# Performance work log

Hardware: AMD Instinct MI355X
Metric: run time of the kernel (lower is better)

## Reference

```python
import jax, jax.numpy as jnp
import numpy as np

# HEAD_ORDER column indices: predictor=0, cf_perm=1, cf_primary=2, cf_secondary=3, reorder=4, interleave=5
# emb rows follow sorted(used_heads) = ['cf_perm','cf_primary','cf_secondary','predictor','reorder']
_HEAD_ROW = {'cf_perm': 0, 'cf_primary': 1, 'cf_secondary': 2, 'predictor': 3, 'reorder': 4}
_HEAD_COL = {'predictor': 0, 'cf_perm': 1, 'cf_primary': 2, 'cf_secondary': 3, 'reorder': 4, 'interleave': 5}
_PAIRS = [('predictor', 'cf_perm'), ('predictor', 'cf_primary'), ('predictor', 'cf_secondary'),
          ('reorder', 'cf_perm'), ('reorder', 'cf_primary'), ('reorder', 'cf_secondary')]
_SCALE = 1.0

BATCH, NEGS, INPUT_DIM, DIM, VOCAB, N_HEADS = 2048, 512, 256, 64, 32, 5


def setup_inputs() -> dict:
    key = jax.random.key(0)
    ks = jax.random.split(key, 5)
    x = jax.random.normal(ks[0], (BATCH, INPUT_DIM), dtype=jnp.float32)
    neg_labels = jax.random.randint(ks[1], (BATCH, NEGS, 6), 0, VOCAB, dtype=jnp.int64)
    emb = jax.random.normal(ks[2], (N_HEADS, VOCAB, DIM), dtype=jnp.float32)
    gate_w = jax.random.normal(ks[3], (6, DIM, INPUT_DIM), dtype=jnp.float32) * (INPUT_DIM ** -0.5)
    gate_b = jax.random.normal(ks[4], (6, DIM), dtype=jnp.float32) * 0.01
    return {'x': x, 'neg_labels': neg_labels, 'emb': emb, 'gate_w': gate_w, 'gate_b': gate_b}


def reference(x, neg_labels, emb, gate_w, gate_b):
    # gates for all 6 pairs at once: (6, batch, dim)
    g = jnp.tanh(jnp.einsum('bi,pdi->pbd', x, gate_w) + gate_b[:, None, :])
    score = jnp.zeros((neg_labels.shape[0], neg_labels.shape[1]), dtype=x.dtype)
    for p, (a, b) in enumerate(_PAIRS):
        ea = emb[_HEAD_ROW[a]][neg_labels[:, :, _HEAD_COL[a]]]  # (batch, negs, dim)
        eb = emb[_HEAD_ROW[b]][neg_labels[:, :, _HEAD_COL[b]]]  # (batch, negs, dim)
        score = score + jnp.einsum('bnd,bd,bnd->bn', ea, g[p], eb)
    return score * _SCALE
```

## Files before the change

kernel.cpp:

```cpp
#include <hip/hip_runtime.h>
#include <hip/hip_bf16.h>

typedef __bf16 bf16x8 __attribute__((ext_vector_type(8)));
typedef float f32x4 __attribute__((ext_vector_type(4)));

#define BATCH 2048
#define NEGS 512
#define IN_DIM 256
#define DIM 64
#define NGATE 384
#define EMB_LD 72
#define TAB_LD 33

__device__ inline bf16x8 cvt8(float4 f0, float4 f1) {
    bf16x8 r;
    r[0] = (__bf16)f0.x; r[1] = (__bf16)f0.y; r[2] = (__bf16)f0.z; r[3] = (__bf16)f0.w;
    r[4] = (__bf16)f1.x; r[5] = (__bf16)f1.y; r[6] = (__bf16)f1.z; r[7] = (__bf16)f1.w;
    return r;
}

__global__ __launch_bounds__(64) void gate_gemm_kernel(
    const float* __restrict__ x, const float* __restrict__ gw,
    const float* __restrict__ gb, float* __restrict__ g)
{
    const int l = threadIdx.x;
    const int lm = l & 15, lq = l >> 4;
    const int m0 = blockIdx.x * 32;
    const int n0 = blockIdx.y * 32;
    f32x4 acc[2][2] = {};

#pragma unroll
    for (int s = 0; s < 8; ++s) {
        const int k0 = s * 32 + lq * 8;
        bf16x8 af[2], bfr[2];
#pragma unroll
        for (int mh = 0; mh < 2; ++mh) {
            const float* p = x + (size_t)(m0 + mh * 16 + lm) * IN_DIM + k0;
            af[mh] = cvt8(*(const float4*)p, *(const float4*)(p + 4));
        }
#pragma unroll
        for (int nh = 0; nh < 2; ++nh) {
            const float* p = gw + (size_t)(n0 + nh * 16 + lm) * IN_DIM + k0;
            bfr[nh] = cvt8(*(const float4*)p, *(const float4*)(p + 4));
        }
#pragma unroll
        for (int mh = 0; mh < 2; ++mh)
#pragma unroll
            for (int nh = 0; nh < 2; ++nh)
                acc[mh][nh] = __builtin_amdgcn_mfma_f32_16x16x32_bf16(af[mh], bfr[nh], acc[mh][nh], 0, 0, 0);
    }

#pragma unroll
    for (int mh = 0; mh < 2; ++mh) {
#pragma unroll
        for (int nh = 0; nh < 2; ++nh) {
            const int gc = n0 + nh * 16 + lm;
            const float bias = gb[gc];
#pragma unroll
            for (int r = 0; r < 4; ++r) {
                const int gr = m0 + mh * 16 + lq * 4 + r;
                g[(size_t)gr * NGATE + gc] = tanhf(acc[mh][nh][r] + bias);
            }
        }
    }
}

__global__ __launch_bounds__(256) void table_score_kernel(
    const int* __restrict__ labels, const float* __restrict__ emb,
    const float* __restrict__ g, float* __restrict__ out)
{
    __shared__ __align__(16) __bf16 embs[5 * 32 * EMB_LD];
    __shared__ __align__(16) float tab[2 * 6 * 32 * TAB_LD];

    const int t = threadIdx.x;
    const int b0 = blockIdx.x * 2;

#pragma unroll
    for (int c = 0; c < 5; ++c) {
        const int j = t + c * 256;
        const int head = j >> 8;
        const int rem = j & 255;
        const int v = rem >> 3, q = rem & 7;
        const float4* src = (const float4*)(emb + (size_t)j * 8);
        bf16x8 val = cvt8(src[0], src[1]);
        *(bf16x8*)&embs[head * (32 * EMB_LD) + v * EMB_LD + q * 8] = val;
    }
    __syncthreads();

    const int w = t >> 6, l = t & 63;
    const int lm = l & 15, lq = l >> 4;

    for (int id = w; id < 12; id += 4) {
        const int bi = id / 6, p = id % 6;
        const int b = b0 + bi;
        const int arow = (p < 3) ? 3 : 4;
        const int crow = (p < 3) ? p : p - 3;
        f32x4 acc[2][2] = {};

#pragma unroll
        for (int s = 0; s < 2; ++s) {
            const int k0 = s * 32 + lq * 8;
            const float* gp = g + (size_t)b * NGATE + p * 64 + k0;
            const float4 g0 = *(const float4*)gp;
            const float4 g1 = *(const float4*)(gp + 4);

            bf16x8 bfr[2], afr[2];
#pragma unroll
            for (int nh = 0; nh < 2; ++nh)
                bfr[nh] = *(const bf16x8*)&embs[crow * (32 * EMB_LD) + (nh * 16 + lm) * EMB_LD + k0];
#pragma unroll
            for (int mh = 0; mh < 2; ++mh) {
                bf16x8 ea = *(const bf16x8*)&embs[arow * (32 * EMB_LD) + (mh * 16 + lm) * EMB_LD + k0];
                bf16x8 r;
                r[0] = (__bf16)((float)ea[0] * g0.x); r[1] = (__bf16)((float)ea[1] * g0.y);
                r[2] = (__bf16)((float)ea[2] * g0.z); r[3] = (__bf16)((float)ea[3] * g0.w);
                r[4] = (__bf16)((float)ea[4] * g1.x); r[5] = (__bf16)((float)ea[5] * g1.y);
                r[6] = (__bf16)((float)ea[6] * g1.z); r[7] = (__bf16)((float)ea[7] * g1.w);
                afr[mh] = r;
            }
#pragma unroll
            for (int mh = 0; mh < 2; ++mh)
#pragma unroll
                for (int nh = 0; nh < 2; ++nh)
                    acc[mh][nh] = __builtin_amdgcn_mfma_f32_16x16x32_bf16(afr[mh], bfr[nh], acc[mh][nh], 0, 0, 0);
        }

        float* tb = tab + id * (32 * TAB_LD);
#pragma unroll
        for (int mh = 0; mh < 2; ++mh)
#pragma unroll
            for (int nh = 0; nh < 2; ++nh) {
                const int col = nh * 16 + lm;
#pragma unroll
                for (int r = 0; r < 4; ++r)
                    tb[(mh * 16 + lq * 4 + r) * TAB_LD + col] = acc[mh][nh][r];
            }
    }
    __syncthreads();

#pragma unroll
    for (int bi = 0; bi < 2; ++bi) {
        const int b = b0 + bi;
        const int4* lp = (const int4*)(labels + (size_t)b * NEGS * 6) + 3 * t;
        const int4 q0 = lp[0];
        const int4 q1 = lp[1];
        const int4 q2 = lp[2];
        const float* tb = tab + bi * (6 * 32 * TAB_LD);

        const float sA =
            tb[0 * 32 * TAB_LD + q0.x * TAB_LD + q0.y] +
            tb[1 * 32 * TAB_LD + q0.x * TAB_LD + q0.z] +
            tb[2 * 32 * TAB_LD + q0.x * TAB_LD + q0.w] +
            tb[3 * 32 * TAB_LD + q1.x * TAB_LD + q0.y] +
            tb[4 * 32 * TAB_LD + q1.x * TAB_LD + q0.z] +
            tb[5 * 32 * TAB_LD + q1.x * TAB_LD + q0.w];
        const float sB =
            tb[0 * 32 * TAB_LD + q1.z * TAB_LD + q1.w] +
            tb[1 * 32 * TAB_LD + q1.z * TAB_LD + q2.x] +
            tb[2 * 32 * TAB_LD + q1.z * TAB_LD + q2.y] +
            tb[3 * 32 * TAB_LD + q2.z * TAB_LD + q1.w] +
            tb[4 * 32 * TAB_LD + q2.z * TAB_LD + q2.x] +
            tb[5 * 32 * TAB_LD + q2.z * TAB_LD + q2.y];

        float2 res; res.x = sA; res.y = sB;
        *(float2*)(out + (size_t)b * NEGS + 2 * t) = res;
    }
}

extern "C" void kernel_launch(void* const* d_in, const int* in_sizes, int n_in,
                              void* d_out, int out_size, void* d_ws, size_t ws_size,
                              hipStream_t stream) {
    const float* x      = (const float*)d_in[0];
    const int*   labels = (const int*)d_in[1];
    const float* emb    = (const float*)d_in[2];
    const float* gw     = (const float*)d_in[3];
    const float* gb     = (const float*)d_in[4];
    float* out = (float*)d_out;
    float* g   = (float*)d_ws;

    hipLaunchKernelGGL(gate_gemm_kernel, dim3(BATCH / 32, NGATE / 32), dim3(64), 0, stream,
                       x, gw, gb, g);
    hipLaunchKernelGGL(table_score_kernel, dim3(BATCH / 2), dim3(256), 0, stream,
                       labels, emb, g, out);
}
```

Measured before the change: 29.72 us.

## Store gates and score tables in bf16, retile gate GEMM, prefetch labels early

The gate GEMM now gives each wave one 16x16 tile, packs four waves per block, and writes the gates as bf16 instead of fp32. The score kernel loads labels and gates into registers before the embedding staging and barrier, so those global loads overlap the shared-memory setup. The per-pair score tables are stored in bf16, halving their LDS footprint, and occupancy is hinted to 3 blocks per CU. This cuts global and LDS traffic but adds bf16 rounding to the gate and table values, and the register prefetch raises register pressure.

Result: faster. 27.12 us (-8.8%).

```diff
diff --git a/kernel.cpp b/kernel.cpp
--- a/kernel.cpp
+++ b/kernel.cpp
@@ -7,10 +7,9 @@
 #define BATCH 2048
 #define NEGS 512
 #define IN_DIM 256
-#define DIM 64
 #define NGATE 384
 #define EMB_LD 72
-#define TAB_LD 33
+#define TAB_LD 34
 
 __device__ inline bf16x8 cvt8(float4 f0, float4 f1) {
     bf16x8 r;
@@ -19,80 +18,78 @@
     return r;
 }
 
-__global__ __launch_bounds__(64) void gate_gemm_kernel(
+__global__ __launch_bounds__(256) void gate_gemm_kernel(
     const float* __restrict__ x, const float* __restrict__ gw,
-    const float* __restrict__ gb, float* __restrict__ g)
+    const float* __restrict__ gb, __bf16* __restrict__ g)
 {
-    const int l = threadIdx.x;
+    const int w = threadIdx.x >> 6, l = threadIdx.x & 63;
     const int lm = l & 15, lq = l >> 4;
-    const int m0 = blockIdx.x * 32;
-    const int n0 = blockIdx.y * 32;
-    f32x4 acc[2][2] = {};
+    const int tile = blockIdx.x * 4 + w;
+    const int mt = tile / 24, nt = tile % 24;
+    const int m0 = mt * 16, n0 = nt * 16;
 
+    const float* xp = x + (size_t)(m0 + lm) * IN_DIM + lq * 8;
+    const float* wp = gw + (size_t)(n0 + lm) * IN_DIM + lq * 8;
+    f32x4 acc = {};
 #pragma unroll
     for (int s = 0; s < 8; ++s) {
-        const int k0 = s * 32 + lq * 8;
-        bf16x8 af[2], bfr[2];
+        bf16x8 a = cvt8(*(const float4*)(xp + s * 32), *(const float4*)(xp + s * 32 + 4));
+        bf16x8 b = cvt8(*(const float4*)(wp + s * 32), *(const float4*)(wp + s * 32 + 4));
+        acc = __builtin_amdgcn_mfma_f32_16x16x32_bf16(a, b, acc, 0, 0, 0);
+    }
+    const int col = n0 + lm;
+    const float bias = gb[col];
 #pragma unroll
-        for (int mh = 0; mh < 2; ++mh) {
-            const float* p = x + (size_t)(m0 + mh * 16 + lm) * IN_DIM + k0;
-            af[mh] = cvt8(*(const float4*)p, *(const float4*)(p + 4));
-        }
-#pragma unroll
-        for (int nh = 0; nh < 2; ++nh) {
-            const float* p = gw + (size_t)(n0 + nh * 16 + lm) * IN_DIM + k0;
-            bfr[nh] = cvt8(*(const float4*)p, *(const float4*)(p + 4));
-        }
-#pragma unroll
-        for (int mh = 0; mh < 2; ++mh)
-#pragma unroll
-            for (int nh = 0; nh < 2; ++nh)
-                acc[mh][nh] = __builtin_amdgcn_mfma_f32_16x16x32_bf16(af[mh], bfr[nh], acc[mh][nh], 0, 0, 0);
-    }
-
-#pragma unroll
-    for (int mh = 0; mh < 2; ++mh) {
-#pragma unroll
-        for (int nh = 0; nh < 2; ++nh) {
-            const int gc = n0 + nh * 16 + lm;
-            const float bias = gb[gc];
-#pragma unroll
-            for (int r = 0; r < 4; ++r) {
-                const int gr = m0 + mh * 16 + lq * 4 + r;
-                g[(size_t)gr * NGATE + gc] = tanhf(acc[mh][nh][r] + bias);
-            }
-        }
+    for (int r = 0; r < 4; ++r) {
+        const int row = m0 + lq * 4 + r;
+        g[(size_t)row * NGATE + col] = (__bf16)tanhf(acc[r] + bias);
     }
 }
 
-__global__ __launch_bounds__(256) void table_score_kernel(
+__global__ __launch_bounds__(256, 3) void table_score_kernel(
     const int* __restrict__ labels, const float* __restrict__ emb,
-    const float* __restrict__ g, float* __restrict__ out)
+    const __bf16* __restrict__ g, float* __restrict__ out)
 {
     __shared__ __align__(16) __bf16 embs[5 * 32 * EMB_LD];
-    __shared__ __align__(16) float tab[2 * 6 * 32 * TAB_LD];
+    __shared__ __align__(16) __bf16 tab[2 * 6 * 32 * TAB_LD];
 
     const int t = threadIdx.x;
     const int b0 = blockIdx.x * 2;
+    const int w = t >> 6, l = t & 63;
+    const int lm = l & 15, lq = l >> 4;
+
+    int4 q[2][3];
+#pragma unroll
+    for (int bi = 0; bi < 2; ++bi) {
+        const int4* lp = (const int4*)(labels + (size_t)(b0 + bi) * NEGS * 6) + 3 * t;
+        q[bi][0] = lp[0]; q[bi][1] = lp[1]; q[bi][2] = lp[2];
+    }
+    bf16x8 gv[3][2];
+#pragma unroll
+    for (int j = 0; j < 3; ++j) {
+        const int id = w + j * 4;
+        const int bi = id / 6, p = id % 6;
+        const __bf16* gp = g + (size_t)(b0 + bi) * NGATE + p * 64 + lq * 8;
+        gv[j][0] = *(const bf16x8*)gp;
+        gv[j][1] = *(const bf16x8*)(gp + 32);
+    }
 
 #pragma unroll
     for (int c = 0; c < 5; ++c) {
         const int j = t + c * 256;
         const int head = j >> 8;
         const int rem = j & 255;
-        const int v = rem >> 3, q = rem & 7;
+        const int v = rem >> 3, qq = rem & 7;
         const float4* src = (const float4*)(emb + (size_t)j * 8);
         bf16x8 val = cvt8(src[0], src[1]);
-        *(bf16x8*)&embs[head * (32 * EMB_LD) + v * EMB_LD + q * 8] = val;
+        *(bf16x8*)&embs[head * (32 * EMB_LD) + v * EMB_LD + qq * 8] = val;
     }
     __syncthreads();
 
-    const int w = t >> 6, l = t & 63;
-    const int lm = l & 15, lq = l >> 4;
-
-    for (int id = w; id < 12; id += 4) {
-        const int bi = id / 6, p = id % 6;
-        const int b = b0 + bi;
+#pragma unroll
+    for (int j = 0; j < 3; ++j) {
+        const int id = w + j * 4;
+        const int p = id % 6;
         const int arow = (p < 3) ? 3 : 4;
         const int crow = (p < 3) ? p : p - 3;
         f32x4 acc[2][2] = {};
@@ -100,9 +97,9 @@
 #pragma unroll
         for (int s = 0; s < 2; ++s) {
             const int k0 = s * 32 + lq * 8;
-            const float* gp = g + (size_t)b * NGATE + p * 64 + k0;
-            const float4 g0 = *(const float4*)gp;
-            const float4 g1 = *(const float4*)(gp + 4);
+            float gf[8];
+#pragma unroll
+            for (int i = 0; i < 8; ++i) gf[i] = (float)gv[j][s][i];
 
             bf16x8 bfr[2], afr[2];
 #pragma unroll
@@ -112,10 +109,8 @@
             for (int mh = 0; mh < 2; ++mh) {
                 bf16x8 ea = *(const bf16x8*)&embs[arow * (32 * EMB_LD) + (mh * 16 + lm) * EMB_LD + k0];
                 bf16x8 r;
-                r[0] = (__bf16)((float)ea[0] * g0.x); r[1] = (__bf16)((float)ea[1] * g0.y);
-                r[2] = (__bf16)((float)ea[2] * g0.z); r[3] = (__bf16)((float)ea[3] * g0.w);
-                r[4] = (__bf16)((float)ea[4] * g1.x); r[5] = (__bf16)((float)ea[5] * g1.y);
-                r[6] = (__bf16)((float)ea[6] * g1.z); r[7] = (__bf16)((float)ea[7] * g1.w);
+#pragma unroll
+                for (int i = 0; i < 8; ++i) r[i] = (__bf16)((float)ea[i] * gf[i]);
                 afr[mh] = r;
             }
 #pragma unroll
@@ -125,7 +120,7 @@
                     acc[mh][nh] = __builtin_amdgcn_mfma_f32_16x16x32_bf16(afr[mh], bfr[nh], acc[mh][nh], 0, 0, 0);
         }
 
-        float* tb = tab + id * (32 * TAB_LD);
+        __bf16* tb = tab + id * (32 * TAB_LD);
 #pragma unroll
         for (int mh = 0; mh < 2; ++mh)
 #pragma unroll
@@ -133,7 +128,7 @@
                 const int col = nh * 16 + lm;
 #pragma unroll
                 for (int r = 0; r < 4; ++r)
-                    tb[(mh * 16 + lq * 4 + r) * TAB_LD + col] = acc[mh][nh][r];
+                    tb[(mh * 16 + lq * 4 + r) * TAB_LD + col] = (__bf16)acc[mh][nh][r];
             }
     }
     __syncthreads();
@@ -141,26 +136,25 @@
 #pragma unroll
     for (int bi = 0; bi < 2; ++bi) {
         const int b = b0 + bi;
-        const int4* lp = (const int4*)(labels + (size_t)b * NEGS * 6) + 3 * t;
-        const int4 q0 = lp[0];
-        const int4 q1 = lp[1];
-        const int4 q2 = lp[2];
-        const float* tb = tab + bi * (6 * 32 * TAB_LD);
+        const int4 q0 = q[bi][0];
+        const int4 q1 = q[bi][1];
+        const int4 q2 = q[bi][2];
+        const __bf16* tb = tab + bi * (6 * 32 * TAB_LD);
 
         const float sA =
-            tb[0 * 32 * TAB_LD + q0.x * TAB_LD + q0.y] +
-            tb[1 * 32 * TAB_LD + q0.x * TAB_LD + q0.z] +
-            tb[2 * 32 * TAB_LD + q0.x * TAB_LD + q0.w] +
-            tb[3 * 32 * TAB_LD + q1.x * TAB_LD + q0.y] +
-            tb[4 * 32 * TAB_LD + q1.x * TAB_LD + q0.z] +
-            tb[5 * 32 * TAB_LD + q1.x * TAB_LD + q0.w];
+            (float)tb[0 * 32 * TAB_LD + q0.x * TAB_LD + q0.y] +
+            (float)tb[1 * 32 * TAB_LD + q0.x * TAB_LD + q0.z] +
+            (float)tb[2 * 32 * TAB_LD + q0.x * TAB_LD + q0.w] +
+            (float)tb[3 * 32 * TAB_LD + q1.x * TAB_LD + q0.y] +
+            (float)tb[4 * 32 * TAB_LD + q1.x * TAB_LD + q0.z] +
+            (float)tb[5 * 32 * TAB_LD + q1.x * TAB_LD + q0.w];
         const float sB =
-            tb[0 * 32 * TAB_LD + q1.z * TAB_LD + q1.w] +
-            tb[1 * 32 * TAB_LD + q1.z * TAB_LD + q2.x] +
-            tb[2 * 32 * TAB_LD + q1.z * TAB_LD + q2.y] +
-            tb[3 * 32 * TAB_LD + q2.z * TAB_LD + q1.w] +
-            tb[4 * 32 * TAB_LD + q2.z * TAB_LD + q2.x] +
-            tb[5 * 32 * TAB_LD + q2.z * TAB_LD + q2.y];
+            (float)tb[0 * 32 * TAB_LD + q1.z * TAB_LD + q1.w] +
+            (float)tb[1 * 32 * TAB_LD + q1.z * TAB_LD + q2.x] +
+            (float)tb[2 * 32 * TAB_LD + q1.z * TAB_LD + q2.y] +
+            (float)tb[3 * 32 * TAB_LD + q2.z * TAB_LD + q1.w] +
+            (float)tb[4 * 32 * TAB_LD + q2.z * TAB_LD + q2.x] +
+            (float)tb[5 * 32 * TAB_LD + q2.z * TAB_LD + q2.y];
 
         float2 res; res.x = sA; res.y = sB;
         *(float2*)(out + (size_t)b * NEGS + 2 * t) = res;
@@ -176,10 +170,9 @@
     const float* gw     = (const float*)d_in[3];
     const float* gb     = (const float*)d_in[4];
     float* out = (float*)d_out;
-    float* g   = (float*)d_ws;
+    __bf16* g  = (__bf16*)d_ws;
 
-    hipLaunchKernelGGL(gate_gemm_kernel, dim3(BATCH / 32, NGATE / 32), dim3(64), 0, stream,
-                       x, gw, gb, g);
+    hipLaunchKernelGGL(gate_gemm_kernel, dim3(768), dim3(256), 0, stream, x, gw, gb, g);
     hipLaunchKernelGGL(table_score_kernel, dim3(BATCH / 2), dim3(256), 0, stream,
                        labels, emb, g, out);
 }
```
